# Performance work log

Hardware: AMD Instinct MI355X
Metric: run time of the kernel (lower is better)

The kernel has to match this reference:

```python
import jax, jax.numpy as jnp
import numpy as np

N_NODES = 50000
N_EDGES = 600000
DIM = 128
N_LAYERS = 4  # input + num_layers(2) hidden + output SAGEConvs


def setup_inputs() -> dict:
    key = jax.random.key(0)
    k_x, k_e, k_wl, k_wr = jax.random.split(key, 4)
    scale = 1.0 / np.sqrt(DIM)
    x = jax.random.normal(k_x, (N_NODES, DIM), dtype=jnp.float32)
    edge_index = jax.random.randint(k_e, (2, N_EDGES), 0, N_NODES, dtype=jnp.int64)
    # Stacked per-layer params: Wl applied to aggregated neighbors (with bias),
    # Wr applied to root features (no bias), matching PyG SAGEConv defaults.
    Wl = jax.random.normal(k_wl, (N_LAYERS, DIM, DIM), dtype=jnp.float32) * scale
    Wr = jax.random.normal(k_wr, (N_LAYERS, DIM, DIM), dtype=jnp.float32) * scale
    b = jnp.zeros((N_LAYERS, DIM), dtype=jnp.float32)
    return {"x": x, "Wl": Wl, "Wr": Wr, "b": b, "edge_index": edge_index}


def reference(x, Wl, Wr, b, edge_index):
    src, dst = edge_index[0], edge_index[1]
    n = x.shape[0]
    ones = jnp.ones((src.shape[0],), dtype=x.dtype)
    deg = jax.ops.segment_sum(ones, dst, num_segments=n)
    inv_deg = 1.0 / jnp.maximum(deg, 1.0)  # [N]; mean with empty-neighborhood -> 0

    def sage_conv(h, W_l, W_r, bias):
        # gather neighbor feats, scatter-mean at destinations
        agg = jax.ops.segment_sum(h[src], dst, num_segments=n) * inv_deg[:, None]
        return jax.nn.relu(agg @ W_l + h @ W_r + bias)

    h = x
    for i in range(Wl.shape[0]):
        h = sage_conv(h, Wl[i], Wr[i], b[i])
    return h
```

## Files before the change

### kernel.cpp

```cpp
#include <hip/hip_runtime.h>

#define N_NODES 50000
#define N_EDGES 600000
#define DIM     128
#define NSB     196

typedef __attribute__((ext_vector_type(8))) short short8b;
typedef __attribute__((ext_vector_type(4))) float f32x4;

__device__ inline unsigned short f2bf(float f) {
    unsigned int u = __builtin_bit_cast(unsigned int, f);
    unsigned int r = (u + 0x7FFFu + ((u >> 16) & 1u)) >> 16;
    return (unsigned short)r;
}
__device__ inline float bf2f(unsigned short b) {
    unsigned int u = ((unsigned int)b) << 16;
    return __builtin_bit_cast(float, u);
}

__global__ void deg_hist_kernel(const int* __restrict__ dst, int* __restrict__ deg) {
    int e = blockIdx.x * blockDim.x + threadIdx.x;
    if (e < N_EDGES) atomicAdd(&deg[dst[e]], 1);
}

__global__ __launch_bounds__(256) void scan_partial_kernel(const int* __restrict__ deg,
                                                           int* __restrict__ part) {
    __shared__ int s[256];
    int t = threadIdx.x;
    int i = blockIdx.x * 256 + t;
    s[t] = (i < N_NODES) ? deg[i] : 0;
    __syncthreads();
    for (int off = 128; off > 0; off >>= 1) {
        if (t < off) s[t] += s[t + off];
        __syncthreads();
    }
    if (t == 0) part[blockIdx.x] = s[0];
}

__global__ __launch_bounds__(256) void scan_offsets_kernel(const int* __restrict__ part,
                                                           int* __restrict__ bofs) {
    __shared__ int s[256];
    int t = threadIdx.x;
    int v = (t < NSB) ? part[t] : 0;
    s[t] = v;
    __syncthreads();
    for (int off = 1; off < 256; off <<= 1) {
        int u = (t >= off) ? s[t - off] : 0;
        __syncthreads();
        s[t] += u;
        __syncthreads();
    }
    bofs[t] = s[t] - v;
}

__global__ __launch_bounds__(256) void scan_final_kernel(const int* __restrict__ deg,
                                                         const int* __restrict__ bofs,
                                                         int* __restrict__ rowptr) {
    __shared__ int s[256];
    int t = threadIdx.x;
    int i = blockIdx.x * 256 + t;
    int v = (i < N_NODES) ? deg[i] : 0;
    s[t] = v;
    __syncthreads();
    for (int off = 1; off < 256; off <<= 1) {
        int u = (t >= off) ? s[t - off] : 0;
        __syncthreads();
        s[t] += u;
        __syncthreads();
    }
    int ex = bofs[blockIdx.x] + s[t] - v;
    if (i < N_NODES) rowptr[i] = ex;
    if (i == N_NODES - 1) rowptr[N_NODES] = ex + v;
}

__global__ void fill_kernel(const int* __restrict__ src, const int* __restrict__ dst,
                            const int* __restrict__ rowptr, int* __restrict__ cursor,
                            int* __restrict__ csr_src) {
    int e = blockIdx.x * blockDim.x + threadIdx.x;
    if (e >= N_EDGES) return;
    int d = dst[e];
    int pos = rowptr[d] + atomicAdd(&cursor[d], 1);
    csr_src[pos] = src[e];
}

__global__ void convert_x_kernel(const float* __restrict__ x, unsigned short* __restrict__ xb) {
    int i = blockIdx.x * blockDim.x + threadIdx.x;
    const float4 v = *(const float4*)&x[(size_t)i * 4];
    ushort4 o;
    o.x = f2bf(v.x); o.y = f2bf(v.y); o.z = f2bf(v.z); o.w = f2bf(v.w);
    *(ushort4*)&xb[(size_t)i * 4] = o;
}

__global__ void prep_w_kernel(const float* __restrict__ Wl, const float* __restrict__ Wr,
                              unsigned short* __restrict__ Bt) {
    int idx = blockIdx.x * blockDim.x + threadIdx.x;
    if (idx >= 4 * 2 * 128 * 128) return;
    int l   = idx >> 15;
    int mat = (idx >> 14) & 1;
    int k   = (idx >> 7) & 127;
    int c   = idx & 127;
    const float* W = mat ? Wr : Wl;
    float w = W[l * 16384 + k * 128 + c];
    unsigned short hi = f2bf(w);
    float res = w - bf2f(hi);
    unsigned short lo = f2bf(res);
    size_t base = ((size_t)(l * 4 + mat * 2) * 128 + c) * 128 + k;
    Bt[base]         = hi;
    Bt[base + 16384] = lo;
}

__global__ __launch_bounds__(256) void gemm_kernel(
    const unsigned short* __restrict__ h,
    const unsigned short* __restrict__ Bt,
    const float* __restrict__ bias,
    unsigned short* __restrict__ y,
    float* __restrict__ z)
{
    int t = threadIdx.x;
    int lane = t & 63, w = t >> 6;
    int r16 = lane & 15, kg = lane >> 4;
    int row0 = blockIdx.x * 64;
    int colbase = w * 32;

    f32x4 accY[4][2], accZ[4][2];
    #pragma unroll
    for (int rt = 0; rt < 4; rt++)
        #pragma unroll
        for (int c = 0; c < 2; c++) {
            accY[rt][c] = (f32x4){0.f, 0.f, 0.f, 0.f};
            accZ[rt][c] = (f32x4){0.f, 0.f, 0.f, 0.f};
        }

    #pragma unroll
    for (int kk = 0; kk < 4; kk++) {
        int k = kg * 8 + kk * 32;
        short8b a[4];
        #pragma unroll
        for (int rt = 0; rt < 4; rt++) {
            int row = min(row0 + rt * 16 + r16, N_NODES - 1);
            a[rt] = *(const short8b*)&h[(size_t)row * DIM + k];
        }
        #pragma unroll
        for (int c = 0; c < 2; c++) {
            size_t bo = (size_t)(colbase + c * 16 + r16) * 128 + k;
            short8b b0 = *(const short8b*)&Bt[bo];
            short8b b1 = *(const short8b*)&Bt[16384 + bo];
            short8b b2 = *(const short8b*)&Bt[32768 + bo];
            short8b b3 = *(const short8b*)&Bt[49152 + bo];
            #pragma unroll
            for (int rt = 0; rt < 4; rt++) {
                accY[rt][c] = __builtin_amdgcn_mfma_f32_16x16x32_bf16(a[rt], b0, accY[rt][c], 0, 0, 0);
                accY[rt][c] = __builtin_amdgcn_mfma_f32_16x16x32_bf16(a[rt], b1, accY[rt][c], 0, 0, 0);
                accZ[rt][c] = __builtin_amdgcn_mfma_f32_16x16x32_bf16(a[rt], b2, accZ[rt][c], 0, 0, 0);
                accZ[rt][c] = __builtin_amdgcn_mfma_f32_16x16x32_bf16(a[rt], b3, accZ[rt][c], 0, 0, 0);
            }
        }
    }

    #pragma unroll
    for (int rt = 0; rt < 4; rt++) {
        #pragma unroll
        for (int c = 0; c < 2; c++) {
            int col = colbase + c * 16 + r16;
            float bb = bias[col];
            #pragma unroll
            for (int j = 0; j < 4; j++) {
                int grow = row0 + rt * 16 + kg * 4 + j;
                if (grow < N_NODES) {
                    y[(size_t)grow * DIM + col] = f2bf(accY[rt][c][j]);
                    z[(size_t)grow * DIM + col] = accZ[rt][c][j] + bb;
                }
            }
        }
    }
}

__global__ __launch_bounds__(256) void gather_kernel(
    const int* __restrict__ rowptr, const int* __restrict__ csr_src,
    const unsigned short* __restrict__ y, const float* __restrict__ z,
    unsigned short* __restrict__ hout_bf, float* __restrict__ out_f32,
    int final_layer)
{
    int lane = threadIdx.x & 63;
    int gw = blockIdx.x * 4 + (threadIdx.x >> 6);
    int stride = gridDim.x * 4;
    int d2 = lane * 2;

    for (int node = gw; node < N_NODES; node += stride) {
        int beg = rowptr[node], end = rowptr[node + 1];
        float a0 = 0.f, a1 = 0.f;
        int i = beg;
        for (; i + 3 < end; i += 4) {
            int s0 = csr_src[i + 0];
            int s1 = csr_src[i + 1];
            int s2 = csr_src[i + 2];
            int s3 = csr_src[i + 3];
            unsigned int u0 = *(const unsigned int*)&y[(size_t)s0 * DIM + d2];
            unsigned int u1 = *(const unsigned int*)&y[(size_t)s1 * DIM + d2];
            unsigned int u2 = *(const unsigned int*)&y[(size_t)s2 * DIM + d2];
            unsigned int u3 = *(const unsigned int*)&y[(size_t)s3 * DIM + d2];
            a0 += __builtin_bit_cast(float, u0 << 16) + __builtin_bit_cast(float, u1 << 16)
                + __builtin_bit_cast(float, u2 << 16) + __builtin_bit_cast(float, u3 << 16);
            a1 += __builtin_bit_cast(float, u0 & 0xffff0000u) + __builtin_bit_cast(float, u1 & 0xffff0000u)
                + __builtin_bit_cast(float, u2 & 0xffff0000u) + __builtin_bit_cast(float, u3 & 0xffff0000u);
        }
        for (; i < end; i++) {
            int s = csr_src[i];
            unsigned int u = *(const unsigned int*)&y[(size_t)s * DIM + d2];
            a0 += __builtin_bit_cast(float, u << 16);
            a1 += __builtin_bit_cast(float, u & 0xffff0000u);
        }
        float sc = 1.0f / fmaxf((float)(end - beg), 1.0f);
        const float2 zz = *(const float2*)&z[(size_t)node * DIM + d2];
        float v0 = fmaxf(a0 * sc + zz.x, 0.f);
        float v1 = fmaxf(a1 * sc + zz.y, 0.f);
        if (final_layer) {
            float2 o = { v0, v1 };
            *(float2*)&out_f32[(size_t)node * DIM + d2] = o;
        } else {
            ushort2 o = { f2bf(v0), f2bf(v1) };
            *(ushort2*)&hout_bf[(size_t)node * DIM + d2] = o;
        }
    }
}

extern "C" void kernel_launch(void* const* d_in, const int* in_sizes, int n_in,
                              void* d_out, int out_size, void* d_ws, size_t ws_size,
                              hipStream_t stream) {
    const float* x  = (const float*)d_in[0];
    const float* Wl = (const float*)d_in[1];
    const float* Wr = (const float*)d_in[2];
    const float* b  = (const float*)d_in[3];
    const int*   ei = (const int*)d_in[4];
    const int* src = ei;
    const int* dst = ei + N_EDGES;
    float* out = (float*)d_out;

    char* ws = (char*)d_ws;
    int* deg     = (int*)(ws + 0);
    int* cursor  = (int*)(ws + 200192);
    int* rowptr  = (int*)(ws + 400384);
    int* csr_src = (int*)(ws + 600592);
    int* part    = (int*)(ws + 3000848);
    int* bofs    = (int*)(ws + 3001872);
    unsigned short* Bt   = (unsigned short*)(ws + 3003136);
    unsigned short* x_bf = (unsigned short*)(ws + 3527680);
    unsigned short* h1   = (unsigned short*)(ws + 16327936);
    unsigned short* ybuf = (unsigned short*)(ws + 29128192);

    hipMemsetAsync(deg, 0, 400384, stream);

    deg_hist_kernel<<<(N_EDGES + 255) / 256, 256, 0, stream>>>(dst, deg);
    scan_partial_kernel<<<NSB, 256, 0, stream>>>(deg, part);
    scan_offsets_kernel<<<1, 256, 0, stream>>>(part, bofs);
    scan_final_kernel<<<NSB, 256, 0, stream>>>(deg, bofs, rowptr);
    fill_kernel<<<(N_EDGES + 255) / 256, 256, 0, stream>>>(src, dst, rowptr, cursor, csr_src);
    convert_x_kernel<<<(N_NODES * DIM / 4 + 255) / 256, 256, 0, stream>>>(x, x_bf);
    prep_w_kernel<<<(4 * 2 * 128 * 128 + 255) / 256, 256, 0, stream>>>(Wl, Wr, Bt);

    const int gemm_blk   = (N_NODES + 63) / 64;
    const int gather_blk = 2048;

    const unsigned short* hin = x_bf;
    unsigned short* houts[4] = { h1, x_bf, h1, nullptr };

    for (int l = 0; l < 4; l++) {
        int fin = (l == 3) ? 1 : 0;
        gemm_kernel<<<gemm_blk, 256, 0, stream>>>(
            hin, Bt + (size_t)l * 4 * 16384, b + (size_t)l * DIM, ybuf, out);
        gather_kernel<<<gather_blk, 256, 0, stream>>>(
            rowptr, csr_src, ybuf, out, houts[l], out, fin);
        hin = houts[l];
    }
}
```

Baseline: 415.5 us.

## Aggregate before transform and merge setup kernels into one launch

Switches the layer order from transform-then-aggregate (GEMM producing a bf16 y plus an fp32 z, then gather) to gather-then-transform. The gather now averages raw bf16 h into an agg buffer, and a single K=256 GEMM over [agg|h] applies bias and ReLU and writes the next h. This removes the fp32 z write and read per layer, at the cost of writing and reading a bf16 agg buffer. It also changes the rounding order, since the mean is rounded to bf16 before the matmul. Separately, the degree histogram, x conversion and weight split/transpose kernels are merged into one launch.

After: 405.2 us. -2.5%, faster.

```diff
diff --git a/kernel.cpp b/kernel.cpp
--- a/kernel.cpp
+++ b/kernel.cpp
@@ -5,6 +5,10 @@
 #define DIM     128
 #define NSB     196
 
+#define HIST_BLKS 2344
+#define CONV_BLKS 3125
+#define PREP_BLKS 512
+
 typedef __attribute__((ext_vector_type(8))) short short8b;
 typedef __attribute__((ext_vector_type(4))) float f32x4;
 
@@ -18,9 +22,36 @@
     return __builtin_bit_cast(float, u);
 }
 
-__global__ void deg_hist_kernel(const int* __restrict__ dst, int* __restrict__ deg) {
-    int e = blockIdx.x * blockDim.x + threadIdx.x;
-    if (e < N_EDGES) atomicAdd(&deg[dst[e]], 1);
+__global__ __launch_bounds__(256) void setup_kernel(
+    const int* __restrict__ dst, int* __restrict__ deg,
+    const float* __restrict__ x, unsigned short* __restrict__ xb,
+    const float* __restrict__ Wl, const float* __restrict__ Wr,
+    unsigned short* __restrict__ Bt) {
+    int b = blockIdx.x, t = threadIdx.x;
+    if (b < HIST_BLKS) {
+        int e = b * 256 + t;
+        if (e < N_EDGES) atomicAdd(&deg[dst[e]], 1);
+    } else if (b < HIST_BLKS + CONV_BLKS) {
+        int i = (b - HIST_BLKS) * 256 + t;
+        size_t base = (size_t)i * 8;
+        const float4 v0 = *(const float4*)&x[base];
+        const float4 v1 = *(const float4*)&x[base + 4];
+        unsigned short o[8] = { f2bf(v0.x), f2bf(v0.y), f2bf(v0.z), f2bf(v0.w),
+                                f2bf(v1.x), f2bf(v1.y), f2bf(v1.z), f2bf(v1.w) };
+        *(short8b*)&xb[base] = *(short8b*)o;
+    } else {
+        int idx = (b - HIST_BLKS - CONV_BLKS) * 256 + t;
+        int l = idx >> 15;
+        int k = (idx & 32767) >> 7;
+        int c = idx & 127;
+        float w = (k < 128) ? Wl[l * 16384 + k * 128 + c]
+                            : Wr[l * 16384 + (k - 128) * 128 + c];
+        unsigned short hi = f2bf(w);
+        unsigned short lo = f2bf(w - bf2f(hi));
+        size_t o = (size_t)l * 65536 + (size_t)c * 256 + k;
+        Bt[o]         = hi;
+        Bt[o + 32768] = lo;
+    }
 }
 
 __global__ __launch_bounds__(256) void scan_partial_kernel(const int* __restrict__ deg,
@@ -83,103 +114,9 @@
     csr_src[pos] = src[e];
 }
 
-__global__ void convert_x_kernel(const float* __restrict__ x, unsigned short* __restrict__ xb) {
-    int i = blockIdx.x * blockDim.x + threadIdx.x;
-    const float4 v = *(const float4*)&x[(size_t)i * 4];
-    ushort4 o;
-    o.x = f2bf(v.x); o.y = f2bf(v.y); o.z = f2bf(v.z); o.w = f2bf(v.w);
-    *(ushort4*)&xb[(size_t)i * 4] = o;
-}
-
-__global__ void prep_w_kernel(const float* __restrict__ Wl, const float* __restrict__ Wr,
-                              unsigned short* __restrict__ Bt) {
-    int idx = blockIdx.x * blockDim.x + threadIdx.x;
-    if (idx >= 4 * 2 * 128 * 128) return;
-    int l   = idx >> 15;
-    int mat = (idx >> 14) & 1;
-    int k   = (idx >> 7) & 127;
-    int c   = idx & 127;
-    const float* W = mat ? Wr : Wl;
-    float w = W[l * 16384 + k * 128 + c];
-    unsigned short hi = f2bf(w);
-    float res = w - bf2f(hi);
-    unsigned short lo = f2bf(res);
-    size_t base = ((size_t)(l * 4 + mat * 2) * 128 + c) * 128 + k;
-    Bt[base]         = hi;
-    Bt[base + 16384] = lo;
-}
-
-__global__ __launch_bounds__(256) void gemm_kernel(
-    const unsigned short* __restrict__ h,
-    const unsigned short* __restrict__ Bt,
-    const float* __restrict__ bias,
-    unsigned short* __restrict__ y,
-    float* __restrict__ z)
-{
-    int t = threadIdx.x;
-    int lane = t & 63, w = t >> 6;
-    int r16 = lane & 15, kg = lane >> 4;
-    int row0 = blockIdx.x * 64;
-    int colbase = w * 32;
-
-    f32x4 accY[4][2], accZ[4][2];
-    #pragma unroll
-    for (int rt = 0; rt < 4; rt++)
-        #pragma unroll
-        for (int c = 0; c < 2; c++) {
-            accY[rt][c] = (f32x4){0.f, 0.f, 0.f, 0.f};
-            accZ[rt][c] = (f32x4){0.f, 0.f, 0.f, 0.f};
-        }
-
-    #pragma unroll
-    for (int kk = 0; kk < 4; kk++) {
-        int k = kg * 8 + kk * 32;
-        short8b a[4];
-        #pragma unroll
-        for (int rt = 0; rt < 4; rt++) {
-            int row = min(row0 + rt * 16 + r16, N_NODES - 1);
-            a[rt] = *(const short8b*)&h[(size_t)row * DIM + k];
-        }
-        #pragma unroll
-        for (int c = 0; c < 2; c++) {
-            size_t bo = (size_t)(colbase + c * 16 + r16) * 128 + k;
-            short8b b0 = *(const short8b*)&Bt[bo];
-            short8b b1 = *(const short8b*)&Bt[16384 + bo];
-            short8b b2 = *(const short8b*)&Bt[32768 + bo];
-            short8b b3 = *(const short8b*)&Bt[49152 + bo];
-            #pragma unroll
-            for (int rt = 0; rt < 4; rt++) {
-                accY[rt][c] = __builtin_amdgcn_mfma_f32_16x16x32_bf16(a[rt], b0, accY[rt][c], 0, 0, 0);
-                accY[rt][c] = __builtin_amdgcn_mfma_f32_16x16x32_bf16(a[rt], b1, accY[rt][c], 0, 0, 0);
-                accZ[rt][c] = __builtin_amdgcn_mfma_f32_16x16x32_bf16(a[rt], b2, accZ[rt][c], 0, 0, 0);
-                accZ[rt][c] = __builtin_amdgcn_mfma_f32_16x16x32_bf16(a[rt], b3, accZ[rt][c], 0, 0, 0);
-            }
-        }
-    }
-
-    #pragma unroll
-    for (int rt = 0; rt < 4; rt++) {
-        #pragma unroll
-        for (int c = 0; c < 2; c++) {
-            int col = colbase + c * 16 + r16;
-            float bb = bias[col];
-            #pragma unroll
-            for (int j = 0; j < 4; j++) {
-                int grow = row0 + rt * 16 + kg * 4 + j;
-                if (grow < N_NODES) {
-                    y[(size_t)grow * DIM + col] = f2bf(accY[rt][c][j]);
-                    z[(size_t)grow * DIM + col] = accZ[rt][c][j] + bb;
-                }
-            }
-        }
-    }
-}
-
 __global__ __launch_bounds__(256) void gather_kernel(
     const int* __restrict__ rowptr, const int* __restrict__ csr_src,
-    const unsigned short* __restrict__ y, const float* __restrict__ z,
-    unsigned short* __restrict__ hout_bf, float* __restrict__ out_f32,
-    int final_layer)
+    const unsigned short* __restrict__ h, unsigned short* __restrict__ agg)
 {
     int lane = threadIdx.x & 63;
     int gw = blockIdx.x * 4 + (threadIdx.x >> 6);
@@ -195,10 +132,10 @@
             int s1 = csr_src[i + 1];
             int s2 = csr_src[i + 2];
             int s3 = csr_src[i + 3];
-            unsigned int u0 = *(const unsigned int*)&y[(size_t)s0 * DIM + d2];
-            unsigned int u1 = *(const unsigned int*)&y[(size_t)s1 * DIM + d2];
-            unsigned int u2 = *(const unsigned int*)&y[(size_t)s2 * DIM + d2];
-            unsigned int u3 = *(const unsigned int*)&y[(size_t)s3 * DIM + d2];
+            unsigned int u0 = *(const unsigned int*)&h[(size_t)s0 * DIM + d2];
+            unsigned int u1 = *(const unsigned int*)&h[(size_t)s1 * DIM + d2];
+            unsigned int u2 = *(const unsigned int*)&h[(size_t)s2 * DIM + d2];
+            unsigned int u3 = *(const unsigned int*)&h[(size_t)s3 * DIM + d2];
             a0 += __builtin_bit_cast(float, u0 << 16) + __builtin_bit_cast(float, u1 << 16)
                 + __builtin_bit_cast(float, u2 << 16) + __builtin_bit_cast(float, u3 << 16);
             a1 += __builtin_bit_cast(float, u0 & 0xffff0000u) + __builtin_bit_cast(float, u1 & 0xffff0000u)
@@ -206,20 +143,76 @@
         }
         for (; i < end; i++) {
             int s = csr_src[i];
-            unsigned int u = *(const unsigned int*)&y[(size_t)s * DIM + d2];
+            unsigned int u = *(const unsigned int*)&h[(size_t)s * DIM + d2];
             a0 += __builtin_bit_cast(float, u << 16);
             a1 += __builtin_bit_cast(float, u & 0xffff0000u);
         }
         float sc = 1.0f / fmaxf((float)(end - beg), 1.0f);
-        const float2 zz = *(const float2*)&z[(size_t)node * DIM + d2];
-        float v0 = fmaxf(a0 * sc + zz.x, 0.f);
-        float v1 = fmaxf(a1 * sc + zz.y, 0.f);
-        if (final_layer) {
-            float2 o = { v0, v1 };
-            *(float2*)&out_f32[(size_t)node * DIM + d2] = o;
-        } else {
-            ushort2 o = { f2bf(v0), f2bf(v1) };
-            *(ushort2*)&hout_bf[(size_t)node * DIM + d2] = o;
+        ushort2 o = { f2bf(a0 * sc), f2bf(a1 * sc) };
+        *(ushort2*)&agg[(size_t)node * DIM + d2] = o;
+    }
+}
+
+__global__ __launch_bounds__(256) void gemm_kernel(
+    const unsigned short* __restrict__ agg,
+    const unsigned short* __restrict__ h,
+    const unsigned short* __restrict__ Bt,
+    const float* __restrict__ bias,
+    unsigned short* __restrict__ out_bf, float* __restrict__ out_f32,
+    int final_layer)
+{
+    int t = threadIdx.x;
+    int lane = t & 63, w = t >> 6;
+    int r16 = lane & 15, kg = lane >> 4;
+    int row0 = blockIdx.x * 64;
+    int colbase = w * 32;
+
+    f32x4 acc[4][2];
+    #pragma unroll
+    for (int rt = 0; rt < 4; rt++)
+        #pragma unroll
+        for (int c = 0; c < 2; c++)
+            acc[rt][c] = (f32x4){0.f, 0.f, 0.f, 0.f};
+
+    #pragma unroll
+    for (int kk = 0; kk < 8; kk++) {
+        int k = kg * 8 + kk * 32;
+        const unsigned short* Ab = (kk < 4) ? agg : h;
+        int kloc = k - ((kk < 4) ? 0 : 128);
+        short8b a[4];
+        #pragma unroll
+        for (int rt = 0; rt < 4; rt++) {
+            int row = min(row0 + rt * 16 + r16, N_NODES - 1);
+            a[rt] = *(const short8b*)&Ab[(size_t)row * DIM + kloc];
+        }
+        #pragma unroll
+        for (int c = 0; c < 2; c++) {
+            size_t bo = (size_t)(colbase + c * 16 + r16) * 256 + k;
+            short8b bh = *(const short8b*)&Bt[bo];
+            short8b bl = *(const short8b*)&Bt[32768 + bo];
+            #pragma unroll
+            for (int rt = 0; rt < 4; rt++) {
+                acc[rt][c] = __builtin_amdgcn_mfma_f32_16x16x32_bf16(a[rt], bh, acc[rt][c], 0, 0, 0);
+                acc[rt][c] = __builtin_amdgcn_mfma_f32_16x16x32_bf16(a[rt], bl, acc[rt][c], 0, 0, 0);
+            }
+        }
+    }
+
+    #pragma unroll
+    for (int rt = 0; rt < 4; rt++) {
+        #pragma unroll
+        for (int c = 0; c < 2; c++) {
+            int col = colbase + c * 16 + r16;
+            float bb = bias[col];
+            #pragma unroll
+            for (int j = 0; j < 4; j++) {
+                int grow = row0 + rt * 16 + kg * 4 + j;
+                if (grow < N_NODES) {
+                    float v = fmaxf(acc[rt][c][j] + bb, 0.f);
+                    if (final_layer) out_f32[(size_t)grow * DIM + col] = v;
+                    else             out_bf [(size_t)grow * DIM + col] = f2bf(v);
+                }
+            }
         }
     }
 }
@@ -245,31 +238,31 @@
     int* bofs    = (int*)(ws + 3001872);
     unsigned short* Bt   = (unsigned short*)(ws + 3003136);
     unsigned short* x_bf = (unsigned short*)(ws + 3527680);
-    unsigned short* h1   = (unsigned short*)(ws + 16327936);
-    unsigned short* ybuf = (unsigned short*)(ws + 29128192);
+    unsigned short* hA   = (unsigned short*)(ws + 16327680);
+    unsigned short* hB   = (unsigned short*)(ws + 29127680);
+    unsigned short* aggb = (unsigned short*)(ws + 41927680);
 
     hipMemsetAsync(deg, 0, 400384, stream);
 
-    deg_hist_kernel<<<(N_EDGES + 255) / 256, 256, 0, stream>>>(dst, deg);
+    setup_kernel<<<HIST_BLKS + CONV_BLKS + PREP_BLKS, 256, 0, stream>>>(
+        dst, deg, x, x_bf, Wl, Wr, Bt);
     scan_partial_kernel<<<NSB, 256, 0, stream>>>(deg, part);
     scan_offsets_kernel<<<1, 256, 0, stream>>>(part, bofs);
     scan_final_kernel<<<NSB, 256, 0, stream>>>(deg, bofs, rowptr);
-    fill_kernel<<<(N_EDGES + 255) / 256, 256, 0, stream>>>(src, dst, rowptr, cursor, csr_src);
-    convert_x_kernel<<<(N_NODES * DIM / 4 + 255) / 256, 256, 0, stream>>>(x, x_bf);
-    prep_w_kernel<<<(4 * 2 * 128 * 128 + 255) / 256, 256, 0, stream>>>(Wl, Wr, Bt);
+    fill_kernel<<<HIST_BLKS, 256, 0, stream>>>(src, dst, rowptr, cursor, csr_src);
 
     const int gemm_blk   = (N_NODES + 63) / 64;
     const int gather_blk = 2048;
 
     const unsigned short* hin = x_bf;
-    unsigned short* houts[4] = { h1, x_bf, h1, nullptr };
+    unsigned short* houts[4] = { hA, hB, hA, nullptr };
 
     for (int l = 0; l < 4; l++) {
         int fin = (l == 3) ? 1 : 0;
+        gather_kernel<<<gather_blk, 256, 0, stream>>>(rowptr, csr_src, hin, aggb);
         gemm_kernel<<<gemm_blk, 256, 0, stream>>>(
-            hin, Bt + (size_t)l * 4 * 16384, b + (size_t)l * DIM, ybuf, out);
-        gather_kernel<<<gather_blk, 256, 0, stream>>>(
-            rowptr, csr_src, ybuf, out, houts[l], out, fin);
+            aggb, hin, Bt + (size_t)l * 65536, b + (size_t)l * DIM,
+            houts[l], out, fin);
         hin = houts[l];
     }
 }
```
